# Performance work log

Hardware: AMD Instinct MI355X
Metric: run time of the kernel (lower is better)

Reference implementation:

```python
import jax, jax.numpy as jnp
import numpy as np

B, T, IN, H = 32, 256, 64, 128
TOP_K = 5
TRUNC = 100   # truncate_length: detach h,c every TRUNC steps
EPS = 1e-7
NEG = -1e9


def setup_inputs() -> dict:
    key = jax.random.key(0)
    ks = jax.random.split(key, 6)
    s = 1.0 / np.sqrt(H)  # torch LSTMCell default init bound
    xav = float(1.414 * np.sqrt(6.0 / (2 * H + 1)))  # xavier_uniform gain=1.414
    return {
        "x": jax.random.normal(ks[0], (B, T, IN), jnp.float32),
        "W_ih": jax.random.uniform(ks[1], (4 * H, IN), jnp.float32, -s, s),
        "W_hh": jax.random.uniform(ks[2], (4 * H, H), jnp.float32, -s, s),
        "b_ih": jax.random.uniform(ks[3], (4 * H,), jnp.float32, -s, s),
        "b_hh": jax.random.uniform(ks[4], (4 * H,), jnp.float32, -s, s),
        "w_t": jax.random.uniform(ks[5], (2 * H, 1), jnp.float32, -xav, xav),
    }


def _lstm_cell(x_t, h, c, W_ih, W_hh, b_ih, b_hh):
    # torch gate order: i, f, g, o
    g = x_t @ W_ih.T + h @ W_hh.T + (b_ih + b_hh)
    i, f, gg, o = jnp.split(g, 4, axis=-1)
    c = jax.nn.sigmoid(f) * c + jax.nn.sigmoid(i) * jnp.tanh(gg)
    h = jax.nn.sigmoid(o) * jnp.tanh(c)
    return h, c


def reference(x, W_ih, W_hh, b_ih, b_hh, w_t):
    Bv, Tv, _ = x.shape
    Hh = W_hh.shape[1]
    # score = w_t . tanh(cat(h_t, h_old)) splits additively since tanh is elementwise
    w_a = w_t[:Hh, 0]
    w_b = w_t[Hh:, 0]
    pos = jnp.arange(Tv + 1)

    def step(carry, inp):
        h, c, h_old = carry          # h_old: [B, T+1, H], slot 0 = initial zeros
        i, x_t = inp
        det = ((i + 1) % TRUNC) == 0
        h = jnp.where(det, jax.lax.stop_gradient(h), h)
        c = jnp.where(det, jax.lax.stop_gradient(c), c)
        h, c = _lstm_cell(x_t, h, c, W_ih, W_hh, b_ih, b_hh)
        rem = i + 1                  # remember_size
        mask = pos < rem             # [T+1] valid memory slots
        # attention scores over stored states
        s = (jnp.tanh(h) @ w_a)[:, None] + jnp.tanh(h_old) @ w_b  # [B, T+1]
        s_valid = jnp.where(mask[None, :], s, NEG)
        delta = jax.lax.top_k(s_valid, TOP_K)[0][:, -1] + EPS
        w_sp = jnp.clip(s_valid - delta[:, None], 0.0)
        w_sp = w_sp / (w_sp.sum(axis=1, keepdims=True) + EPS)
        # Sparse_attention returns raw scores when remember_size <= top_k
        attn_w = jnp.where(rem <= TOP_K, s, w_sp)
        attn_c = jnp.einsum('bt,bth->bh', jnp.where(mask[None, :], attn_w, 0.0), h_old)
        h = h + attn_c
        h_old = jax.lax.dynamic_update_slice(h_old, h[:, None, :], (0, rem, 0))
        return (h, c, h_old), (attn_c, attn_w)

    h0 = jnp.zeros((Bv, Hh), x.dtype)
    c0 = jnp.zeros((Bv, Hh), x.dtype)
    buf0 = jnp.zeros((Bv, Tv + 1, Hh), x.dtype)
    xs = (jnp.arange(Tv), jnp.swapaxes(x, 0, 1))
    _, (attn_c_all, attn_w_all) = jax.lax.scan(step, (h0, c0, buf0), xs)
    # module returns last step's (attn_c, out_attn_w); final remember_size == T
    return attn_c_all[-1], attn_w_all[-1][:, :Tv, None]
```

## Files before the change

### kernel.cpp

```cpp
#include <hip/hip_runtime.h>
#include <math.h>

#define NEGF -1000000000.0f
#define EPSF 1e-7f


#define RAWBAR() asm volatile("s_waitcnt lgkmcnt(0)\n\ts_barrier" ::: "memory")

__device__ __forceinline__ float fsigmoid(float x) {
  return 1.0f / (1.0f + __expf(-x));
}
__device__ __forceinline__ float ftanh(float x) {
  return 1.0f - 2.0f / (1.0f + __expf(2.0f * x));
}

__device__ __forceinline__ float wave_allsum(float v) {
#if __has_builtin(__builtin_amdgcn_update_dpp) && __has_builtin(__builtin_amdgcn_readlane)
  float f = v;
#define DPPSTEP(ctrl, rmask) { \
    int t = __builtin_amdgcn_update_dpp(0, __builtin_bit_cast(int, f), \
                                        ctrl, rmask, 0xf, true); \
    f += __builtin_bit_cast(float, t); }
  DPPSTEP(0x111, 0xf)
  DPPSTEP(0x112, 0xf)
  DPPSTEP(0x114, 0xf)
  DPPSTEP(0x118, 0xf)
  DPPSTEP(0x142, 0xa)
  DPPSTEP(0x143, 0x8)
#undef DPPSTEP
  return __builtin_bit_cast(float,
      __builtin_amdgcn_readlane(__builtin_bit_cast(int, f), 63));
#else
  for (int off = 1; off < 64; off <<= 1) v += __shfl_xor(v, off, 64);
  return v;
#endif
}

__global__ __launch_bounds__(512) void xw_kernel(
    const float* __restrict__ x, const float* __restrict__ W_ih,
    const float* __restrict__ b_ih, const float* __restrict__ b_hh,
    float* __restrict__ xw)
{
  const int t0 = blockIdx.x * 32;
  const int b  = blockIdx.y;
  const int g  = threadIdx.x;

  __shared__ float sx[32 * 64];
  ((float4*)sx)[threadIdx.x] =
      ((const float4*)(x + (size_t)(b * 256 + t0) * 64))[threadIdx.x];

  const float4* wr = (const float4*)(W_ih + (size_t)g * 64);
  float4 w0 = wr[0],  w1 = wr[1],  w2 = wr[2],  w3 = wr[3],
         w4 = wr[4],  w5 = wr[5],  w6 = wr[6],  w7 = wr[7],
         w8 = wr[8],  w9 = wr[9],  w10 = wr[10], w11 = wr[11],
         w12 = wr[12], w13 = wr[13], w14 = wr[14], w15 = wr[15];
  const float bias = b_ih[g] + b_hh[g];
  __syncthreads();

  float* dst = xw + (size_t)(b * 256 + t0) * 512 + g;
  for (int tt = 0; tt < 32; ++tt) {
    const float4* xr = (const float4*)(sx + tt * 64);
    float a0 = 0.0f, a1 = 0.0f, a2 = 0.0f, a3 = 0.0f;
#define XSTEP(j) { float4 hv = xr[j]; \
    a0 = fmaf(w##j.x, hv.x, a0); a1 = fmaf(w##j.y, hv.y, a1); \
    a2 = fmaf(w##j.z, hv.z, a2); a3 = fmaf(w##j.w, hv.w, a3); }
    XSTEP(0) XSTEP(1) XSTEP(2) XSTEP(3) XSTEP(4) XSTEP(5) XSTEP(6) XSTEP(7)
    XSTEP(8) XSTEP(9) XSTEP(10) XSTEP(11) XSTEP(12) XSTEP(13) XSTEP(14) XSTEP(15)
#undef XSTEP
    dst[(size_t)tt * 512] = (a0 + a1) + (a2 + a3) + bias;
  }
}

__global__
__attribute__((amdgpu_flat_work_group_size(1024, 1024), amdgpu_waves_per_eu(4, 4)))
void lstm_attn(
    const float* __restrict__ xw, const float* __restrict__ W_hh,
    const float* __restrict__ w_t, float* __restrict__ out)
{
  const int b   = blockIdx.x;
  const int tid = threadIdx.x;
  const int l   = tid & 63;
  const int wid = tid >> 6;
  const int p   = tid & 255;
  const int q   = tid >> 8;
  const int gA  = p;
  const int gB  = p + 256;

  __shared__ float ho[257 * 128];
  __shared__ float sh_part[4 * 512];
  __shared__ float sh_d[8];

  const float4* pA = (const float4*)(W_hh + (size_t)gA * 128 + (q << 5));
  const float4* pB = (const float4*)(W_hh + (size_t)gB * 128 + (q << 5));
  float4 wA0 = pA[0], wA1 = pA[1], wA2 = pA[2], wA3 = pA[3],
         wA4 = pA[4], wA5 = pA[5], wA6 = pA[6], wA7 = pA[7];
  float4 wB0 = pB[0], wB1 = pB[1], wB2 = pB[2], wB3 = pB[3],
         wB4 = pB[4], wB5 = pB[5], wB6 = pB[6], wB7 = pB[7];

  const int j0 = 2 * l, j1 = 2 * l + 1;
  float c0 = 0.0f, c1 = 0.0f;
  float wa0 = 0.0f, wa1 = 0.0f, wb0 = 0.0f, wb1 = 0.0f;
  float t5v0 = 0.0f, t5v1 = NEGF, t5v2 = NEGF, t5v3 = NEGF, t5v4 = NEGF;
  int   t5i0 = 0, t5i1 = 0, t5i2 = 0, t5i3 = 0;
  float gn0 = 0.0f, gn1 = 0.0f, gn2 = 0.0f, gn3 = 0.0f;
  int   ofs0 = 0, ofs1 = 0, ofs2 = 0, ofs3 = 0;

  if (wid == 0) {
    wa0 = w_t[j0];       wa1 = w_t[j1];
    wb0 = w_t[128 + j0]; wb1 = w_t[128 + j1];
    *(float2*)(ho + j0) = make_float2(0.0f, 0.0f);
    __builtin_amdgcn_s_setprio(1);
  }
  if (tid == 0) sh_d[0] = 0.0f;
  __syncthreads();

  const float* xwb = xw + (size_t)b * 256 * 512;
  float xcurA = 0.0f, xcurB = 0.0f;
  if (q == 0) { xcurA = xwb[gA]; xcurB = xwb[gB]; }

  for (int i = 0; i < 256; ++i) {
    const int rem = i + 1;
    float hn0 = 0.0f, hn1 = 0.0f;

    float aA0 = xcurA, aA1 = 0.0f, aB0 = xcurB, aB1 = 0.0f;
    if (q == 0 && i < 255) {
      xcurA = xwb[(size_t)(i + 1) * 512 + gA];
      xcurB = xwb[(size_t)(i + 1) * 512 + gB];
    }
    const float4* hh4 = (const float4*)(ho + i * 128 + (q << 5));
#define LSTEP(j) { float4 hv = hh4[j]; \
    aA0 = fmaf(wA##j.x, hv.x, aA0); aA1 = fmaf(wA##j.y, hv.y, aA1); \
    aA0 = fmaf(wA##j.z, hv.z, aA0); aA1 = fmaf(wA##j.w, hv.w, aA1); \
    aB0 = fmaf(wB##j.x, hv.x, aB0); aB1 = fmaf(wB##j.y, hv.y, aB1); \
    aB0 = fmaf(wB##j.z, hv.z, aB0); aB1 = fmaf(wB##j.w, hv.w, aB1); }
    LSTEP(0) LSTEP(1) LSTEP(2) LSTEP(3) LSTEP(4) LSTEP(5) LSTEP(6) LSTEP(7)
#undef LSTEP
    sh_part[(q << 9) + gA] = aA0 + aA1;
    sh_part[(q << 9) + gB] = aB0 + aB1;

    float2 hv0, hv1, hv2, hv3;
    if (wid == 0 && i >= 5) {
      hv0 = *(const float2*)(ho + ofs0);
      hv1 = *(const float2*)(ho + ofs1);
      hv2 = *(const float2*)(ho + ofs2);
      hv3 = *(const float2*)(ho + ofs3);
    }
    RAWBAR();

    if (wid == 0) {
#define GSUM(base) ({ \
      float2 x0 = ((const float2*)(sh_part        + (base)))[l]; \
      float2 x1 = ((const float2*)(sh_part +  512 + (base)))[l]; \
      float2 x2 = ((const float2*)(sh_part + 1024 + (base)))[l]; \
      float2 x3 = ((const float2*)(sh_part + 1536 + (base)))[l]; \
      float2 r; r.x = (x0.x + x1.x) + (x2.x + x3.x); \
      r.y = (x0.y + x1.y) + (x2.y + x3.y); r; })
      float2 Pi = GSUM(0), Pf = GSUM(128), Pg = GSUM(256), Po = GSUM(384);
#undef GSUM
      c0 = fsigmoid(Pf.x) * c0 + fsigmoid(Pi.x) * ftanh(Pg.x);
      c1 = fsigmoid(Pf.y) * c1 + fsigmoid(Pi.y) * ftanh(Pg.y);
      float hc0 = fsigmoid(Po.x) * ftanh(c0);
      float hc1 = fsigmoid(Po.y) * ftanh(c1);

      float at0, at1;
      if (i >= 5) {
        at0 = gn0 * hv0.x;            at1 = gn0 * hv0.y;
        at0 = fmaf(gn1, hv1.x, at0);  at1 = fmaf(gn1, hv1.y, at1);
        at0 = fmaf(gn2, hv2.x, at0);  at1 = fmaf(gn2, hv2.y, at1);
        at0 = fmaf(gn3, hv3.x, at0);  at1 = fmaf(gn3, hv3.y, at1);
      } else {
        float a = wave_allsum(ftanh(hc0) * wa0 + ftanh(hc1) * wa1);
        at0 = 0.0f; at1 = 0.0f;
        for (int t = 0; t <= i; ++t) {
          float s = a + sh_d[t];
          float2 hv = *(const float2*)(ho + t * 128 + j0);
          at0 = fmaf(s, hv.x, at0);
          at1 = fmaf(s, hv.y, at1);
        }
      }
      hn0 = hc0 + at0; hn1 = hc1 + at1;
      *(float2*)(ho + rem * 128 + j0) = make_float2(hn0, hn1);
      if (i == 255) {
        out[b * 128 + j0] = at0; out[b * 128 + j1] = at1;
        #pragma unroll
        for (int m = 0; m < 4; ++m) {
          int t = l + 64 * m;
          float val = 0.0f;
          if (t == t5i0) val = gn0;
          if (t == t5i1) val = gn1;
          if (t == t5i2) val = gn2;
          if (t == t5i3) val = gn3;
          out[4096 + b * 256 + t] = val;
        }
      }
    }
    RAWBAR();

    if (wid == 0 && i < 255) {
      float dn = wave_allsum(ftanh(hn0) * wb0 + ftanh(hn1) * wb1);
      if (l == 0 && i < 4) sh_d[rem] = dn;
      float v = dn; int vi = rem;
      if (v > t5v0) { float tv = t5v0; int ti = t5i0; t5v0 = v; t5i0 = vi; v = tv; vi = ti; }
      if (v > t5v1) { float tv = t5v1; int ti = t5i1; t5v1 = v; t5i1 = vi; v = tv; vi = ti; }
      if (v > t5v2) { float tv = t5v2; int ti = t5i2; t5v2 = v; t5i2 = vi; v = tv; vi = ti; }
      if (v > t5v3) { float tv = t5v3; int ti = t5i3; t5v3 = v; t5i3 = vi; v = tv; vi = ti; }
      if (v > t5v4) { t5v4 = v; }
      float g0 = fmaxf(t5v0 - t5v4 - EPSF, 0.0f);
      float g1 = fmaxf(t5v1 - t5v4 - EPSF, 0.0f);
      float g2 = fmaxf(t5v2 - t5v4 - EPSF, 0.0f);
      float g3 = fmaxf(t5v3 - t5v4 - EPSF, 0.0f);
      float inv = 1.0f / (((g0 + g1) + (g2 + g3)) + EPSF);
      gn0 = g0 * inv; gn1 = g1 * inv; gn2 = g2 * inv; gn3 = g3 * inv;
      ofs0 = (t5i0 << 7) + j0; ofs1 = (t5i1 << 7) + j0;
      ofs2 = (t5i2 << 7) + j0; ofs3 = (t5i3 << 7) + j0;
    }
  }
}

extern "C" void kernel_launch(void* const* d_in, const int* in_sizes, int n_in,
                              void* d_out, int out_size, void* d_ws, size_t ws_size,
                              hipStream_t stream) {
  const float* x    = (const float*)d_in[0];
  const float* W_ih = (const float*)d_in[1];
  const float* W_hh = (const float*)d_in[2];
  const float* b_ih = (const float*)d_in[3];
  const float* b_hh = (const float*)d_in[4];
  const float* w_t  = (const float*)d_in[5];
  float* out = (float*)d_out;

  float* xw = (float*)d_ws;

  xw_kernel<<<dim3(8, 32), 512, 0, stream>>>(x, W_ih, b_ih, b_hh, xw);
  lstm_attn<<<dim3(32), 1024, 0, stream>>>(xw, W_hh, w_t, out);
}
```

Baseline: 415.3 us.

## Repartition recurrent matvec into 4 gates by 8 k-slices per thread

The W_hh matvec work is redistributed so each thread handles 4 consecutive gate rows over a 16-wide slice of the hidden vector, instead of 2 rows over a 32-wide slice. Each LDS read of h is reused across four rows, and partial sums go out as one float4 store. The reduction now sums 8 partial buffers instead of 4, which adds LDS traffic for the serial gate-combining wave. Separately, xw_kernel drops its shared-memory staging of x and reads x directly from global memory.

```diff
diff --git a/kernel.cpp b/kernel.cpp
--- a/kernel.cpp
+++ b/kernel.cpp
@@ -45,21 +45,16 @@
   const int b  = blockIdx.y;
   const int g  = threadIdx.x;
 
-  __shared__ float sx[32 * 64];
-  ((float4*)sx)[threadIdx.x] =
-      ((const float4*)(x + (size_t)(b * 256 + t0) * 64))[threadIdx.x];
-
   const float4* wr = (const float4*)(W_ih + (size_t)g * 64);
   float4 w0 = wr[0],  w1 = wr[1],  w2 = wr[2],  w3 = wr[3],
          w4 = wr[4],  w5 = wr[5],  w6 = wr[6],  w7 = wr[7],
          w8 = wr[8],  w9 = wr[9],  w10 = wr[10], w11 = wr[11],
          w12 = wr[12], w13 = wr[13], w14 = wr[14], w15 = wr[15];
   const float bias = b_ih[g] + b_hh[g];
-  __syncthreads();
 
   float* dst = xw + (size_t)(b * 256 + t0) * 512 + g;
   for (int tt = 0; tt < 32; ++tt) {
-    const float4* xr = (const float4*)(sx + tt * 64);
+    const float4* xr = (const float4*)(x + (size_t)(b * 256 + t0 + tt) * 64);
     float a0 = 0.0f, a1 = 0.0f, a2 = 0.0f, a3 = 0.0f;
 #define XSTEP(j) { float4 hv = xr[j]; \
     a0 = fmaf(w##j.x, hv.x, a0); a1 = fmaf(w##j.y, hv.y, a1); \
@@ -81,21 +76,20 @@
   const int tid = threadIdx.x;
   const int l   = tid & 63;
   const int wid = tid >> 6;
-  const int p   = tid & 255;
-  const int q   = tid >> 8;
-  const int gA  = p;
-  const int gB  = p + 256;
+  const int m   = wid >> 3;
+  const int k   = wid & 7;
+  const int g0  = m * 256 + (l << 2);
 
   __shared__ float ho[257 * 128];
-  __shared__ float sh_part[4 * 512];
+  __shared__ float sh_part[8 * 512];
   __shared__ float sh_d[8];
 
-  const float4* pA = (const float4*)(W_hh + (size_t)gA * 128 + (q << 5));
-  const float4* pB = (const float4*)(W_hh + (size_t)gB * 128 + (q << 5));
-  float4 wA0 = pA[0], wA1 = pA[1], wA2 = pA[2], wA3 = pA[3],
-         wA4 = pA[4], wA5 = pA[5], wA6 = pA[6], wA7 = pA[7];
-  float4 wB0 = pB[0], wB1 = pB[1], wB2 = pB[2], wB3 = pB[3],
-         wB4 = pB[4], wB5 = pB[5], wB6 = pB[6], wB7 = pB[7];
+#define LOADW(j) \
+  const float4* pw##j = (const float4*)(W_hh + (size_t)(g0 + j) * 128 + (k << 4)); \
+  float4 w##j##_0 = pw##j[0], w##j##_1 = pw##j[1], \
+         w##j##_2 = pw##j[2], w##j##_3 = pw##j[3];
+  LOADW(0) LOADW(1) LOADW(2) LOADW(3)
+#undef LOADW
 
   const int j0 = 2 * l, j1 = 2 * l + 1;
   float c0 = 0.0f, c1 = 0.0f;
@@ -115,28 +109,30 @@
   __syncthreads();
 
   const float* xwb = xw + (size_t)b * 256 * 512;
-  float xcurA = 0.0f, xcurB = 0.0f;
-  if (q == 0) { xcurA = xwb[gA]; xcurB = xwb[gB]; }
+  float4 xc = make_float4(0.f, 0.f, 0.f, 0.f);
+  if (k == 0) xc = *(const float4*)(xwb + g0);
 
   for (int i = 0; i < 256; ++i) {
     const int rem = i + 1;
     float hn0 = 0.0f, hn1 = 0.0f;
 
-    float aA0 = xcurA, aA1 = 0.0f, aB0 = xcurB, aB1 = 0.0f;
-    if (q == 0 && i < 255) {
-      xcurA = xwb[(size_t)(i + 1) * 512 + gA];
-      xcurB = xwb[(size_t)(i + 1) * 512 + gB];
-    }
-    const float4* hh4 = (const float4*)(ho + i * 128 + (q << 5));
-#define LSTEP(j) { float4 hv = hh4[j]; \
-    aA0 = fmaf(wA##j.x, hv.x, aA0); aA1 = fmaf(wA##j.y, hv.y, aA1); \
-    aA0 = fmaf(wA##j.z, hv.z, aA0); aA1 = fmaf(wA##j.w, hv.w, aA1); \
-    aB0 = fmaf(wB##j.x, hv.x, aB0); aB1 = fmaf(wB##j.y, hv.y, aB1); \
-    aB0 = fmaf(wB##j.z, hv.z, aB0); aB1 = fmaf(wB##j.w, hv.w, aB1); }
-    LSTEP(0) LSTEP(1) LSTEP(2) LSTEP(3) LSTEP(4) LSTEP(5) LSTEP(6) LSTEP(7)
-#undef LSTEP
-    sh_part[(q << 9) + gA] = aA0 + aA1;
-    sh_part[(q << 9) + gB] = aB0 + aB1;
+    float a0x = xc.x, a0y = 0.0f, a1x = xc.y, a1y = 0.0f;
+    float a2x = xc.z, a2y = 0.0f, a3x = xc.w, a3y = 0.0f;
+    if (k == 0 && i < 255)
+      xc = *(const float4*)(xwb + (size_t)(i + 1) * 512 + g0);
+    const float4* hh4 = (const float4*)(ho + i * 128 + (k << 4));
+#define FGA(j, kk) \
+    a##j##x = fmaf(w##j##_##kk.x, hv.x, a##j##x); \
+    a##j##y = fmaf(w##j##_##kk.y, hv.y, a##j##y); \
+    a##j##x = fmaf(w##j##_##kk.z, hv.z, a##j##x); \
+    a##j##y = fmaf(w##j##_##kk.w, hv.w, a##j##y);
+#define KSTEP(kk) { float4 hv = hh4[kk]; \
+    FGA(0, kk) FGA(1, kk) FGA(2, kk) FGA(3, kk) }
+    KSTEP(0) KSTEP(1) KSTEP(2) KSTEP(3)
+#undef KSTEP
+#undef FGA
+    *(float4*)(sh_part + (k << 9) + g0) =
+        make_float4(a0x + a0y, a1x + a1y, a2x + a2y, a3x + a3y);
 
     float2 hv0, hv1, hv2, hv3;
     if (wid == 0 && i >= 5) {
@@ -149,12 +145,18 @@
 
     if (wid == 0) {
 #define GSUM(base) ({ \
-      float2 x0 = ((const float2*)(sh_part        + (base)))[l]; \
-      float2 x1 = ((const float2*)(sh_part +  512 + (base)))[l]; \
-      float2 x2 = ((const float2*)(sh_part + 1024 + (base)))[l]; \
-      float2 x3 = ((const float2*)(sh_part + 1536 + (base)))[l]; \
-      float2 r; r.x = (x0.x + x1.x) + (x2.x + x3.x); \
-      r.y = (x0.y + x1.y) + (x2.y + x3.y); r; })
+      float2 x0 = ((const float2*)(sh_part          + (base)))[l]; \
+      float2 x1 = ((const float2*)(sh_part +  512   + (base)))[l]; \
+      float2 x2 = ((const float2*)(sh_part + 1024   + (base)))[l]; \
+      float2 x3 = ((const float2*)(sh_part + 1536   + (base)))[l]; \
+      float2 x4 = ((const float2*)(sh_part + 2048   + (base)))[l]; \
+      float2 x5 = ((const float2*)(sh_part + 2560   + (base)))[l]; \
+      float2 x6 = ((const float2*)(sh_part + 3072   + (base)))[l]; \
+      float2 x7 = ((const float2*)(sh_part + 3584   + (base)))[l]; \
+      float2 r; \
+      r.x = ((x0.x + x1.x) + (x2.x + x3.x)) + ((x4.x + x5.x) + (x6.x + x7.x)); \
+      r.y = ((x0.y + x1.y) + (x2.y + x3.y)) + ((x4.y + x5.y) + (x6.y + x7.y)); \
+      r; })
       float2 Pi = GSUM(0), Pf = GSUM(128), Pg = GSUM(256), Po = GSUM(384);
 #undef GSUM
       c0 = fsigmoid(Pf.x) * c0 + fsigmoid(Pi.x) * ftanh(Pg.x);
@@ -183,8 +185,8 @@
       if (i == 255) {
         out[b * 128 + j0] = at0; out[b * 128 + j1] = at1;
         #pragma unroll
-        for (int m = 0; m < 4; ++m) {
-          int t = l + 64 * m;
+        for (int mm = 0; mm < 4; ++mm) {
+          int t = l + 64 * mm;
           float val = 0.0f;
           if (t == t5i0) val = gn0;
           if (t == t5i1) val = gn1;
@@ -205,12 +207,12 @@
       if (v > t5v2) { float tv = t5v2; int ti = t5i2; t5v2 = v; t5i2 = vi; v = tv; vi = ti; }
       if (v > t5v3) { float tv = t5v3; int ti = t5i3; t5v3 = v; t5i3 = vi; v = tv; vi = ti; }
       if (v > t5v4) { t5v4 = v; }
-      float g0 = fmaxf(t5v0 - t5v4 - EPSF, 0.0f);
-      float g1 = fmaxf(t5v1 - t5v4 - EPSF, 0.0f);
-      float g2 = fmaxf(t5v2 - t5v4 - EPSF, 0.0f);
-      float g3 = fmaxf(t5v3 - t5v4 - EPSF, 0.0f);
-      float inv = 1.0f / (((g0 + g1) + (g2 + g3)) + EPSF);
-      gn0 = g0 * inv; gn1 = g1 * inv; gn2 = g2 * inv; gn3 = g3 * inv;
+      float g0f = fmaxf(t5v0 - t5v4 - EPSF, 0.0f);
+      float g1f = fmaxf(t5v1 - t5v4 - EPSF, 0.0f);
+      float g2f = fmaxf(t5v2 - t5v4 - EPSF, 0.0f);
+      float g3f = fmaxf(t5v3 - t5v4 - EPSF, 0.0f);
+      float inv = 1.0f / (((g0f + g1f) + (g2f + g3f)) + EPSF);
+      gn0 = g0f * inv; gn1 = g1f * inv; gn2 = g2f * inv; gn3 = g3f * inv;
       ofs0 = (t5i0 << 7) + j0; ofs1 = (t5i1 << 7) + j0;
       ofs2 = (t5i2 << 7) + j0; ofs3 = (t5i3 << 7) + j0;
     }
```

Measured after the change: 518.3 us. +24.8%, slower.

## Fuse input projection into recurrent kernel with flag-based producer/consumer chunks and fp16 xw

Applied to the files above, without the earlier changes.

Merges the separate input-projection kernel into the recurrent kernel launch. Extra blocks compute x·W_ih+bias in 64-step chunks, store it as fp16, and publish release flags. The recurrent blocks spin-wait on each chunk's flag, so the projection overlaps the start of the recurrence and one kernel launch is removed. The risks are fp16 rounding of the gate pre-activations, the added memset launch, and a possible deadlock if producer blocks are not scheduled alongside the spinning consumers.

```diff
diff --git a/kernel.cpp b/kernel.cpp
--- a/kernel.cpp
+++ b/kernel.cpp
@@ -1,4 +1,5 @@
 #include <hip/hip_runtime.h>
+#include <hip/hip_fp16.h>
 #include <math.h>
 
 #define NEGF -1000000000.0f
@@ -36,49 +37,54 @@
 #endif
 }
 
-__global__ __launch_bounds__(512) void xw_kernel(
-    const float* __restrict__ x, const float* __restrict__ W_ih,
-    const float* __restrict__ b_ih, const float* __restrict__ b_hh,
-    float* __restrict__ xw)
-{
-  const int t0 = blockIdx.x * 32;
-  const int b  = blockIdx.y;
-  const int g  = threadIdx.x;
-
-  __shared__ float sx[32 * 64];
-  ((float4*)sx)[threadIdx.x] =
-      ((const float4*)(x + (size_t)(b * 256 + t0) * 64))[threadIdx.x];
-
-  const float4* wr = (const float4*)(W_ih + (size_t)g * 64);
-  float4 w0 = wr[0],  w1 = wr[1],  w2 = wr[2],  w3 = wr[3],
-         w4 = wr[4],  w5 = wr[5],  w6 = wr[6],  w7 = wr[7],
-         w8 = wr[8],  w9 = wr[9],  w10 = wr[10], w11 = wr[11],
-         w12 = wr[12], w13 = wr[13], w14 = wr[14], w15 = wr[15];
-  const float bias = b_ih[g] + b_hh[g];
-  __syncthreads();
-
-  float* dst = xw + (size_t)(b * 256 + t0) * 512 + g;
-  for (int tt = 0; tt < 32; ++tt) {
-    const float4* xr = (const float4*)(sx + tt * 64);
-    float a0 = 0.0f, a1 = 0.0f, a2 = 0.0f, a3 = 0.0f;
-#define XSTEP(j) { float4 hv = xr[j]; \
-    a0 = fmaf(w##j.x, hv.x, a0); a1 = fmaf(w##j.y, hv.y, a1); \
-    a2 = fmaf(w##j.z, hv.z, a2); a3 = fmaf(w##j.w, hv.w, a3); }
-    XSTEP(0) XSTEP(1) XSTEP(2) XSTEP(3) XSTEP(4) XSTEP(5) XSTEP(6) XSTEP(7)
-    XSTEP(8) XSTEP(9) XSTEP(10) XSTEP(11) XSTEP(12) XSTEP(13) XSTEP(14) XSTEP(15)
-#undef XSTEP
-    dst[(size_t)tt * 512] = (a0 + a1) + (a2 + a3) + bias;
-  }
-}
-
 __global__
 __attribute__((amdgpu_flat_work_group_size(1024, 1024), amdgpu_waves_per_eu(4, 4)))
 void lstm_attn(
-    const float* __restrict__ xw, const float* __restrict__ W_hh,
-    const float* __restrict__ w_t, float* __restrict__ out)
+    const float* __restrict__ x, const float* __restrict__ W_ih,
+    const float* __restrict__ W_hh, const float* __restrict__ b_ih,
+    const float* __restrict__ b_hh, const float* __restrict__ w_t,
+    __half* __restrict__ xwh, int* __restrict__ flags,
+    float* __restrict__ out)
 {
+  const int tid = threadIdx.x;
+
+  if (blockIdx.x >= 32) {
+    const int j  = blockIdx.x - 32;
+    const int bb = j >> 2;
+    const int t0 = (j & 3) << 6;
+    const int g  = tid & 511;
+    const int th = tid >> 9;
+
+    const float4* wr = (const float4*)(W_ih + (size_t)g * 64);
+    float4 w0 = wr[0],  w1 = wr[1],  w2 = wr[2],  w3 = wr[3],
+           w4 = wr[4],  w5 = wr[5],  w6 = wr[6],  w7 = wr[7],
+           w8 = wr[8],  w9 = wr[9],  w10 = wr[10], w11 = wr[11],
+           w12 = wr[12], w13 = wr[13], w14 = wr[14], w15 = wr[15];
+    const float bias = b_ih[g] + b_hh[g];
+
+    const int tbase = bb * 256 + t0 + th * 32;
+    __half* dst = xwh + (size_t)tbase * 512 + g;
+    for (int tt = 0; tt < 32; ++tt) {
+      const float4* xr = (const float4*)(x + (size_t)(tbase + tt) * 64);
+      float a0 = 0.0f, a1 = 0.0f, a2 = 0.0f, a3 = 0.0f;
+#define XSTEP(q) { float4 hv = xr[q]; \
+      a0 = fmaf(w##q.x, hv.x, a0); a1 = fmaf(w##q.y, hv.y, a1); \
+      a2 = fmaf(w##q.z, hv.z, a2); a3 = fmaf(w##q.w, hv.w, a3); }
+      XSTEP(0) XSTEP(1) XSTEP(2) XSTEP(3) XSTEP(4) XSTEP(5) XSTEP(6) XSTEP(7)
+      XSTEP(8) XSTEP(9) XSTEP(10) XSTEP(11) XSTEP(12) XSTEP(13) XSTEP(14) XSTEP(15)
+#undef XSTEP
+      dst[(size_t)tt * 512] = __float2half((a0 + a1) + (a2 + a3) + bias);
+    }
+    __syncthreads();
+    if (tid == 0) {
+      __threadfence();
+      __hip_atomic_store(&flags[j], 1, __ATOMIC_RELEASE,
+                         __HIP_MEMORY_SCOPE_AGENT);
+    }
+    return;
+  }
+
   const int b   = blockIdx.x;
-  const int tid = threadIdx.x;
   const int l   = tid & 63;
   const int wid = tid >> 6;
   const int p   = tid & 255;
@@ -114,18 +120,33 @@
   if (tid == 0) sh_d[0] = 0.0f;
   __syncthreads();
 
-  const float* xwb = xw + (size_t)b * 256 * 512;
+#define WAITCHUNK(c) { \
+    if (tid == 0) { \
+      while (__hip_atomic_load(&flags[(b << 2) + (c)], __ATOMIC_ACQUIRE, \
+                               __HIP_MEMORY_SCOPE_AGENT) == 0) \
+        __builtin_amdgcn_s_sleep(8); \
+    } \
+    __syncthreads(); }
+
+  WAITCHUNK(0)
+
+  const __half* xwb = xwh + (size_t)b * 256 * 512;
   float xcurA = 0.0f, xcurB = 0.0f;
-  if (q == 0) { xcurA = xwb[gA]; xcurB = xwb[gB]; }
+  if (q == 0) {
+    xcurA = __half2float(xwb[gA]);
+    xcurB = __half2float(xwb[gB]);
+  }
 
   for (int i = 0; i < 256; ++i) {
     const int rem = i + 1;
     float hn0 = 0.0f, hn1 = 0.0f;
 
+    if ((i & 63) == 63 && i < 255) WAITCHUNK((i + 1) >> 6)
+
     float aA0 = xcurA, aA1 = 0.0f, aB0 = xcurB, aB1 = 0.0f;
     if (q == 0 && i < 255) {
-      xcurA = xwb[(size_t)(i + 1) * 512 + gA];
-      xcurB = xwb[(size_t)(i + 1) * 512 + gB];
+      xcurA = __half2float(xwb[(size_t)(i + 1) * 512 + gA]);
+      xcurB = __half2float(xwb[(size_t)(i + 1) * 512 + gB]);
     }
     const float4* hh4 = (const float4*)(ho + i * 128 + (q << 5));
 #define LSTEP(j) { float4 hv = hh4[j]; \
@@ -228,8 +249,10 @@
   const float* w_t  = (const float*)d_in[5];
   float* out = (float*)d_out;
 
-  float* xw = (float*)d_ws;
-
-  xw_kernel<<<dim3(8, 32), 512, 0, stream>>>(x, W_ih, b_ih, b_hh, xw);
-  lstm_attn<<<dim3(32), 1024, 0, stream>>>(xw, W_hh, w_t, out);
-}
+  __half* xwh = (__half*)d_ws;
+  int* flags  = (int*)((char*)d_ws + 8 * 1024 * 1024);
+
+  hipMemsetAsync(flags, 0, 128 * sizeof(int), stream);
+  lstm_attn<<<dim3(160), 1024, 0, stream>>>(x, W_ih, W_hh, b_ih, b_hh,
+                                            w_t, xwh, flags, out);
+}
```

Result: slower. 659.0 us (+58.7%).

## Halve LSTM block to 512 threads with four gate rows per thread

Applied to the files above, without the earlier changes.

Reduces the recurrent kernel's block from 1024 to 512 threads, so each thread holds four W_hh rows (one per gate) for its k-slice instead of two. This halves the number of waves synchronising at each per-step barrier and the per-step thread count. In exchange each thread runs a longer dependent FMA chain per step and holds more registers, which may raise per-step latency.

```diff
diff --git a/kernel.cpp b/kernel.cpp
--- a/kernel.cpp
+++ b/kernel.cpp
@@ -72,7 +72,7 @@
 }
 
 __global__
-__attribute__((amdgpu_flat_work_group_size(1024, 1024), amdgpu_waves_per_eu(4, 4)))
+__attribute__((amdgpu_flat_work_group_size(512, 512), amdgpu_waves_per_eu(2, 2)))
 void lstm_attn(
     const float* __restrict__ xw, const float* __restrict__ W_hh,
     const float* __restrict__ w_t, float* __restrict__ out)
@@ -81,21 +81,25 @@
   const int tid = threadIdx.x;
   const int l   = tid & 63;
   const int wid = tid >> 6;
-  const int p   = tid & 255;
-  const int q   = tid >> 8;
-  const int gA  = p;
-  const int gB  = p + 256;
+  const int p   = tid & 127;
+  const int q   = tid >> 7;
 
   __shared__ float ho[257 * 128];
   __shared__ float sh_part[4 * 512];
   __shared__ float sh_d[8];
 
-  const float4* pA = (const float4*)(W_hh + (size_t)gA * 128 + (q << 5));
-  const float4* pB = (const float4*)(W_hh + (size_t)gB * 128 + (q << 5));
-  float4 wA0 = pA[0], wA1 = pA[1], wA2 = pA[2], wA3 = pA[3],
-         wA4 = pA[4], wA5 = pA[5], wA6 = pA[6], wA7 = pA[7];
-  float4 wB0 = pB[0], wB1 = pB[1], wB2 = pB[2], wB3 = pB[3],
-         wB4 = pB[4], wB5 = pB[5], wB6 = pB[6], wB7 = pB[7];
+  const float4* pI = (const float4*)(W_hh + (size_t)(p      ) * 128 + (q << 5));
+  const float4* pF = (const float4*)(W_hh + (size_t)(p + 128) * 128 + (q << 5));
+  const float4* pG = (const float4*)(W_hh + (size_t)(p + 256) * 128 + (q << 5));
+  const float4* pO = (const float4*)(W_hh + (size_t)(p + 384) * 128 + (q << 5));
+  float4 wI0 = pI[0], wI1 = pI[1], wI2 = pI[2], wI3 = pI[3],
+         wI4 = pI[4], wI5 = pI[5], wI6 = pI[6], wI7 = pI[7];
+  float4 wF0 = pF[0], wF1 = pF[1], wF2 = pF[2], wF3 = pF[3],
+         wF4 = pF[4], wF5 = pF[5], wF6 = pF[6], wF7 = pF[7];
+  float4 wG0 = pG[0], wG1 = pG[1], wG2 = pG[2], wG3 = pG[3],
+         wG4 = pG[4], wG5 = pG[5], wG6 = pG[6], wG7 = pG[7];
+  float4 wO0 = pO[0], wO1 = pO[1], wO2 = pO[2], wO3 = pO[3],
+         wO4 = pO[4], wO5 = pO[5], wO6 = pO[6], wO7 = pO[7];
 
   const int j0 = 2 * l, j1 = 2 * l + 1;
   float c0 = 0.0f, c1 = 0.0f;
@@ -115,28 +119,41 @@
   __syncthreads();
 
   const float* xwb = xw + (size_t)b * 256 * 512;
-  float xcurA = 0.0f, xcurB = 0.0f;
-  if (q == 0) { xcurA = xwb[gA]; xcurB = xwb[gB]; }
+  float xcI = 0.0f, xcF = 0.0f, xcG = 0.0f, xcO = 0.0f;
+  if (q == 0) {
+    xcI = xwb[p];       xcF = xwb[p + 128];
+    xcG = xwb[p + 256]; xcO = xwb[p + 384];
+  }
 
   for (int i = 0; i < 256; ++i) {
     const int rem = i + 1;
     float hn0 = 0.0f, hn1 = 0.0f;
 
-    float aA0 = xcurA, aA1 = 0.0f, aB0 = xcurB, aB1 = 0.0f;
+    float aI = xcI, aF = xcF, aG = xcG, aO = xcO;
     if (q == 0 && i < 255) {
-      xcurA = xwb[(size_t)(i + 1) * 512 + gA];
-      xcurB = xwb[(size_t)(i + 1) * 512 + gB];
+      const float* xn = xwb + (size_t)(i + 1) * 512;
+      xcI = xn[p];       xcF = xn[p + 128];
+      xcG = xn[p + 256]; xcO = xn[p + 384];
     }
     const float4* hh4 = (const float4*)(ho + i * 128 + (q << 5));
-#define LSTEP(j) { float4 hv = hh4[j]; \
-    aA0 = fmaf(wA##j.x, hv.x, aA0); aA1 = fmaf(wA##j.y, hv.y, aA1); \
-    aA0 = fmaf(wA##j.z, hv.z, aA0); aA1 = fmaf(wA##j.w, hv.w, aA1); \
-    aB0 = fmaf(wB##j.x, hv.x, aB0); aB1 = fmaf(wB##j.y, hv.y, aB1); \
-    aB0 = fmaf(wB##j.z, hv.z, aB0); aB1 = fmaf(wB##j.w, hv.w, aB1); }
-    LSTEP(0) LSTEP(1) LSTEP(2) LSTEP(3) LSTEP(4) LSTEP(5) LSTEP(6) LSTEP(7)
-#undef LSTEP
-    sh_part[(q << 9) + gA] = aA0 + aA1;
-    sh_part[(q << 9) + gB] = aB0 + aB1;
+#define KS(k) { float4 hv = hh4[k]; \
+    aI = fmaf(wI##k.x, hv.x, aI); aI = fmaf(wI##k.y, hv.y, aI); \
+    aI = fmaf(wI##k.z, hv.z, aI); aI = fmaf(wI##k.w, hv.w, aI); \
+    aF = fmaf(wF##k.x, hv.x, aF); aF = fmaf(wF##k.y, hv.y, aF); \
+    aF = fmaf(wF##k.z, hv.z, aF); aF = fmaf(wF##k.w, hv.w, aF); \
+    aG = fmaf(wG##k.x, hv.x, aG); aG = fmaf(wG##k.y, hv.y, aG); \
+    aG = fmaf(wG##k.z, hv.z, aG); aG = fmaf(wG##k.w, hv.w, aG); \
+    aO = fmaf(wO##k.x, hv.x, aO); aO = fmaf(wO##k.y, hv.y, aO); \
+    aO = fmaf(wO##k.z, hv.z, aO); aO = fmaf(wO##k.w, hv.w, aO); }
+    KS(0) KS(1) KS(2) KS(3) KS(4) KS(5) KS(6) KS(7)
+#undef KS
+    {
+      float* sp = sh_part + (q << 9) + p;
+      sp[0]   = aI;
+      sp[128] = aF;
+      sp[256] = aG;
+      sp[384] = aO;
+    }
 
     float2 hv0, hv1, hv2, hv3;
     if (wid == 0 && i >= 5) {
@@ -231,5 +248,5 @@
   float* xw = (float*)d_ws;
 
   xw_kernel<<<dim3(8, 32), 512, 0, stream>>>(x, W_ih, b_ih, b_hh, xw);
-  lstm_attn<<<dim3(32), 1024, 0, stream>>>(xw, W_hh, w_t, out);
-}
+  lstm_attn<<<dim3(32), 512, 0, stream>>>(xw, W_hh, w_t, out);
+}
```

Result: faster. 398.1 us (-4.1%).
